# Kernel optimization log

Measured on AMD Instinct MI355X. Metric: run time of the kernel, lower is better.

## Reference

```python
import jax, jax.numpy as jnp
import numpy as np

HIDDEN = 512
HEADS = 8
HEAD_DIM = HIDDEN // HEADS  # 64
NUM_FEATURES = 256
EPS = 1e-4


def _gaussian_orthogonal_random_matrix(num_rows, num_cols, scaling=0, seed=1234):
    """Blocks of orthogonal rows from QR of gaussian matrices, rescaled (FAVOR+)."""
    rng = np.random.default_rng(seed)
    blocks = []
    full_blocks = num_rows // num_cols
    for _ in range(full_blocks):
        q, _ = np.linalg.qr(rng.standard_normal((num_cols, num_cols)))
        blocks.append(q.T)
    rem = num_rows - full_blocks * num_cols
    if rem > 0:
        q, _ = np.linalg.qr(rng.standard_normal((num_cols, num_cols)))
        blocks.append(q.T[:rem])
    mat = np.concatenate(blocks, axis=0)  # [num_rows, num_cols]
    if scaling == 0:
        # row norms of a fresh gaussian matrix (chi-distributed multipliers)
        multiplier = np.linalg.norm(rng.standard_normal((num_rows, num_cols)), axis=1)
    else:
        multiplier = np.sqrt(num_cols) * np.ones(num_rows)
    return (multiplier[:, None] * mat).astype(np.float32)


def _split_heads(x, b):
    # [b, n, hidden] -> [b, h, n, head_dim]
    return x.reshape(b, -1, HEADS, HEAD_DIM).transpose(0, 2, 1, 3)


def _phi(data, proj):
    """Nonnegative softmax kernel feature map (FAVOR+).
    data: [b,h,n,d], proj: [m,d] -> [b,h,n,m]"""
    d = data.shape[-1]
    m = proj.shape[0]
    x = data * (d ** -0.25)
    dash = jnp.einsum('bhnd,md->bhnm', x, proj)
    diag = 0.5 * jnp.sum(x * x, axis=-1, keepdims=True)
    return (m ** -0.5) * jnp.exp(dash - diag) + EPS


def setup_inputs() -> dict:
    key = jax.random.key(0)
    ks = jax.random.split(key, 12)
    b, n = 2, 8192
    s = HIDDEN ** -0.5
    inp = {
        'query': jax.random.normal(ks[0], (b, n, HIDDEN), jnp.float32),
        'key':   jax.random.normal(ks[1], (b, n, HIDDEN), jnp.float32),
        'value': jax.random.normal(ks[2], (b, n, HIDDEN), jnp.float32),
        'WQ_w': jax.random.normal(ks[3], (HIDDEN, HIDDEN), jnp.float32) * s,
        'WQ_b': jnp.zeros((HIDDEN,), jnp.float32),
        'WK_w': jax.random.normal(ks[4], (HIDDEN, HIDDEN), jnp.float32) * s,
        'WK_b': jnp.zeros((HIDDEN,), jnp.float32),
        'WV_w': jax.random.normal(ks[5], (HIDDEN, HIDDEN), jnp.float32) * s,
        'WV_b': jnp.zeros((HIDDEN,), jnp.float32),
        'WO_w': jax.random.normal(ks[6], (HIDDEN, HIDDEN), jnp.float32) * s,
        'WO_b': jnp.zeros((HIDDEN,), jnp.float32),
        'proj': jnp.asarray(_gaussian_orthogonal_random_matrix(NUM_FEATURES, HEAD_DIM)),
    }
    return inp


def reference(query, key, value, WQ_w, WQ_b, WK_w, WK_b, WV_w, WV_b, WO_w, WO_b, proj):
    b = query.shape[0]
    # torch Linear: y = x @ W.T + b
    Q = _split_heads(jnp.einsum('bnd,ed->bne', query, WQ_w) + WQ_b, b)
    K = _split_heads(jnp.einsum('bnd,ed->bne', key,   WK_w) + WK_b, b)
    V = _split_heads(jnp.einsum('bnd,ed->bne', value, WV_w) + WV_b, b)

    Qp = _phi(Q, proj)  # [b,h,n,m]
    Kp = _phi(K, proj)  # [b,h,n,m]

    # denominator: Q' @ sum_n K'  -> [b,h,n,1]
    denom = jnp.einsum('bhnm,bhm->bhn', Qp, jnp.sum(Kp, axis=2))[..., None]
    # linear attention: Q' @ (K'^T V), O(n*m*d)
    ctx = jnp.einsum('bhnm,bhnd->bhmd', Kp, V)
    attn = jnp.einsum('bhnm,bhmd->bhnd', Qp, ctx) / denom

    # faithful to original: .view(batch, -1, hidden) directly on [b,h,n,d]
    attn = attn.reshape(b, -1, HIDDEN)
    return jnp.einsum('bnd,ed->bne', attn, WO_w) + WO_b
```

## Files before the change

kernel.cpp:

```cpp
#include <hip/hip_runtime.h>

typedef __attribute__((ext_vector_type(8))) _Float16 f16x8;
typedef __attribute__((ext_vector_type(4))) float f32x4;

#define S4 0.35355339059327373f

static __device__ __forceinline__ ushort f2h(float f) {
  return __builtin_bit_cast(ushort, (_Float16)f);
}

static __device__ __forceinline__ void gload16(const void* g, void* l) {
  __builtin_amdgcn_global_load_lds((const __attribute__((address_space(1))) void*)g,
                                   (__attribute__((address_space(3))) void*)l, 16, 0, 0);
}

static __device__ __forceinline__ void cvt_store8(ushort* dst, float4 a, float4 b) {
  f16x8 h;
  h[0] = (_Float16)a.x; h[1] = (_Float16)a.y; h[2] = (_Float16)a.z; h[3] = (_Float16)a.w;
  h[4] = (_Float16)b.x; h[5] = (_Float16)b.y; h[6] = (_Float16)b.z; h[7] = (_Float16)b.w;
  *(f16x8*)dst = h;
}

template<int BM, int BN, int WR, int WC, int EPI, int ZMODE, int DIAG, int AF32, int BF32>
__global__ __launch_bounds__(256) void gemm_bt(
    const void* __restrict__ Av, const void* __restrict__ Bv,
    const float* __restrict__ bias, ushort* __restrict__ Cb,
    float* __restrict__ Cf, const float* __restrict__ rv0,
    float* __restrict__ dg,
    int K, int ldA, int ldB, int ldC, int Mz,
    long sAz, long sBz, long sCz)
{
  constexpr int BK = 32;
  constexpr int WTM = BM / WR, WTN = BN / WC;
  constexpr int MI = WTM / 16, NI = WTN / 16;
  constexpr int LDSB = (BM + BN) * 64;

  __shared__ uint4 smem4[LDSB / 16];
  char* smem = (char*)smem4;
  ushort* As = (ushort*)smem;
  ushort* Bs = (ushort*)(smem + BM * 64);

  const int tid = threadIdx.x;
  const int l = tid & 63, w = tid >> 6;
  const int wr = w / WC, wc = w % WC;
  const int lr = l & 15, lk = l >> 4;
  const int tm = blockIdx.x * BM, tn = blockIdx.y * BN;
  const int z = blockIdx.z;

  const ushort* Ah = (const ushort*)Av;
  const ushort* Bh = (const ushort*)Bv;
  const float*  Af = (const float*)Av;
  const float*  Bf = (const float*)Bv;
  long aoff = 0, boff = 0;
  if (ZMODE == 0) { aoff = (long)z * sAz; boff = (long)z * sBz; }
  if (ZMODE == 1) { aoff = (long)(z >> 3) * sAz + (z & 7) * 64; boff = (long)z * sBz; }
  Ah += aoff; Bh += boff; Af += aoff; Bf += boff;
  const float* rv = (EPI == 1) ? (rv0 + (long)z * Mz) : nullptr;
  const long coff = (long)z * sCz;

  f32x4 acc[MI][NI];
#pragma unroll
  for (int i = 0; i < MI; ++i)
#pragma unroll
    for (int j = 0; j < NI; ++j) acc[i][j] = f32x4{0.f, 0.f, 0.f, 0.f};

  for (int k0 = 0; k0 < K; k0 += BK) {
    if constexpr (AF32) {
      const int ar = tid >> 1, ac = (tid & 1) * 16;
      const float* g = Af + (long)(tm + ar) * ldA + k0 + ac;
      float4 f0 = *(const float4*)(g);
      float4 f1 = *(const float4*)(g + 4);
      float4 f2 = *(const float4*)(g + 8);
      float4 f3 = *(const float4*)(g + 12);
      cvt_store8(As + ar * 32 + ac, f0, f1);
      cvt_store8(As + ar * 32 + ac + 8, f2, f3);
    } else {
      constexpr int AB = BM * 64;
#pragma unroll
      for (int s = 0; s < (AB + 4095) / 4096; ++s) {
        const int base = s * 4096 + w * 1024;
        if (base < AB) {
          const int idx = base + l * 16;
          gload16(Ah + (long)(tm + (idx >> 6)) * ldA + k0 + ((idx & 63) >> 1),
                  (char*)As + base);
        }
      }
    }
    if constexpr (BF32) {
      const int br = tid >> 1, bc = (tid & 1) * 16;
      const float* g = Bf + (long)(tn + br) * ldB + k0 + bc;
      float4 f0 = *(const float4*)(g);
      float4 f1 = *(const float4*)(g + 4);
      float4 f2 = *(const float4*)(g + 8);
      float4 f3 = *(const float4*)(g + 12);
      cvt_store8(Bs + br * 32 + bc, f0, f1);
      cvt_store8(Bs + br * 32 + bc + 8, f2, f3);
    } else {
      constexpr int BB = BN * 64;
#pragma unroll
      for (int s = 0; s < (BB + 4095) / 4096; ++s) {
        const int base = s * 4096 + w * 1024;
        if (base < BB) {
          const int idx = base + l * 16;
          gload16(Bh + (long)(tn + (idx >> 6)) * ldB + k0 + ((idx & 63) >> 1),
                  (char*)Bs + base);
        }
      }
    }
    __syncthreads();

    f16x8 af[MI], bfr[NI];
#pragma unroll
    for (int mi = 0; mi < MI; ++mi)
      af[mi] = *(const f16x8*)(As + (wr * WTM + mi * 16 + lr) * 32 + lk * 8);
#pragma unroll
    for (int ni = 0; ni < NI; ++ni)
      bfr[ni] = *(const f16x8*)(Bs + (wc * WTN + ni * 16 + lr) * 32 + lk * 8);
#pragma unroll
    for (int mi = 0; mi < MI; ++mi)
#pragma unroll
      for (int ni = 0; ni < NI; ++ni)
        acc[mi][ni] = __builtin_amdgcn_mfma_f32_16x16x32_f16(af[mi], bfr[ni], acc[mi][ni], 0, 0, 0);
    __syncthreads();
  }

#pragma unroll
  for (int mi = 0; mi < MI; ++mi) {
#pragma unroll
    for (int j = 0; j < 4; ++j) {
      const int row = tm + wr * WTM + mi * 16 + lk * 4 + j;
      float ds = 0.f;
#pragma unroll
      for (int ni = 0; ni < NI; ++ni) {
        const int col = tn + wc * WTN + ni * 16 + lr;
        float v = acc[mi][ni][j];
        if (EPI == 0 || EPI == 3) v += bias[col];
        if (EPI == 4) v += bias[row];
        if (EPI == 1) v = 0.0625f * __expf(v - rv[row]) + 1e-4f;
        if (DIAG) ds += v * v;
        if (EPI == 4) {
          const int b = col >> 13, nn = col & 8191;
          const int h = row >> 6, d = row & 63;
          Cb[(long)(b * 8 + h) * 655360 + (long)d * 8192 + nn] = f2h(v);
        } else if (EPI == 3) {
          Cf[coff + (long)row * ldC + col] = v;
        } else {
          Cb[coff + (long)row * ldC + col] = f2h(v);
        }
      }
      if (DIAG) {
        ds += __shfl_xor(ds, 1, 64);
        ds += __shfl_xor(ds, 2, 64);
        ds += __shfl_xor(ds, 4, 64);
        ds += __shfl_xor(ds, 8, 64);
        if (lr == 0) {
          const int b = row >> 13, nn = row & 8191;
          const int head = (tn + wc * WTN) >> 6;
          dg[(long)(b * 8 + head) * 8192 + nn] = 0.0625f * ds;
        }
      }
    }
  }
}

__global__ __launch_bounds__(256) void phictx_k(
    const ushort* __restrict__ Kh, const ushort* __restrict__ Vt,
    const ushort* __restrict__ pjh, const float* __restrict__ diagK,
    float* __restrict__ cpart)
{
  const int by = blockIdx.x, z = blockIdx.y;
  const int kc = z >> 4, bh = z & 15;
  const int b = bh >> 3, h = bh & 7;
  const int n0c = kc * 1024;
  const int tid = threadIdx.x, l = tid & 63, w = tid >> 6;
  const int lr = l & 15, lk = l >> 4;

  __shared__ char smem[39680];
  ushort* Pj = (ushort*)smem;
  ushort* Ks = (ushort*)(smem + 18432);
  ushort* Vs = (ushort*)(smem + 23040);
  ushort* Kp = (ushort*)(smem + 29440);

  {
    const ushort* src = pjh + by * 128 * 64;
#pragma unroll
    for (int c = tid; c < 1024; c += 256) {
      const int row = c >> 3, cole = (c & 7) * 8;
      *(uint4*)(Pj + row * 72 + cole) = *(const uint4*)(src + row * 64 + cole);
    }
  }
  const ushort* KB = Kh + (long)b * 4194304 + h * 64;
  const ushort* VB = Vt + (long)bh * 655360;
  const float* rv = diagK + (long)bh * 8192;

  f32x4 acc[5][2];
#pragma unroll
  for (int i = 0; i < 5; ++i) {
    acc[i][0] = f32x4{0.f, 0.f, 0.f, 0.f};
    acc[i][1] = f32x4{0.f, 0.f, 0.f, 0.f};
  }

  for (int ns = 0; ns < 32; ++ns) {
    const int n0 = n0c + ns * 32;
    {
      const int row = tid >> 3, cole = (tid & 7) * 8;
      uint4 u = *(const uint4*)(KB + (long)(n0 + row) * 512 + cole);
      *(uint4*)(Ks + row * 72 + cole) = u;
    }
    {
#pragma unroll
      for (int c = tid; c < 320; c += 256) {
        const int row = c >> 2, cole = (c & 3) * 8;
        uint4 u = *(const uint4*)(VB + (long)row * 8192 + n0 + cole);
        *(uint4*)(Vs + row * 40 + cole) = u;
      }
    }
    __syncthreads();

    f32x4 a2[2][2];
    a2[0][0] = f32x4{0.f,0.f,0.f,0.f}; a2[0][1] = f32x4{0.f,0.f,0.f,0.f};
    a2[1][0] = f32x4{0.f,0.f,0.f,0.f}; a2[1][1] = f32x4{0.f,0.f,0.f,0.f};
#pragma unroll
    for (int kk = 0; kk < 2; ++kk) {
      f16x8 pa[2], kb[2];
#pragma unroll
      for (int mi = 0; mi < 2; ++mi)
        pa[mi] = *(const f16x8*)(Pj + (w * 32 + mi * 16 + lr) * 72 + kk * 32 + lk * 8);
#pragma unroll
      for (int ni = 0; ni < 2; ++ni)
        kb[ni] = *(const f16x8*)(Ks + (ni * 16 + lr) * 72 + kk * 32 + lk * 8);
#pragma unroll
      for (int mi = 0; mi < 2; ++mi)
#pragma unroll
        for (int ni = 0; ni < 2; ++ni)
          a2[mi][ni] = __builtin_amdgcn_mfma_f32_16x16x32_f16(pa[mi], kb[ni], a2[mi][ni], 0, 0, 0);
    }
#pragma unroll
    for (int mi = 0; mi < 2; ++mi)
#pragma unroll
      for (int ni = 0; ni < 2; ++ni)
#pragma unroll
        for (int j = 0; j < 4; ++j) {
          const int mrow = w * 32 + mi * 16 + lk * 4 + j;
          const int ncol = ni * 16 + lr;
          const float vv = 0.0625f * __expf(a2[mi][ni][j] - rv[n0 + ncol]) + 1e-4f;
          Kp[mrow * 40 + ncol] = f2h(vv);
        }
    __syncthreads();

    f16x8 va[5], kb2[2];
#pragma unroll
    for (int mi = 0; mi < 5; ++mi)
      va[mi] = *(const f16x8*)(Vs + (mi * 16 + lr) * 40 + lk * 8);
#pragma unroll
    for (int ni = 0; ni < 2; ++ni)
      kb2[ni] = *(const f16x8*)(Kp + (w * 32 + ni * 16 + lr) * 40 + lk * 8);
#pragma unroll
    for (int mi = 0; mi < 5; ++mi)
#pragma unroll
      for (int ni = 0; ni < 2; ++ni)
        acc[mi][ni] = __builtin_amdgcn_mfma_f32_16x16x32_f16(va[mi], kb2[ni], acc[mi][ni], 0, 0, 0);
    __syncthreads();
  }

  float* out = cpart + (long)z * 20480;
#pragma unroll
  for (int mi = 0; mi < 5; ++mi)
#pragma unroll
    for (int ni = 0; ni < 2; ++ni)
#pragma unroll
      for (int j = 0; j < 4; ++j) {
        const int row = mi * 16 + lk * 4 + j;
        const int col = by * 128 + w * 32 + ni * 16 + lr;
        out[(long)row * 256 + col] = acc[mi][ni][j];
      }
}

__global__ __launch_bounds__(256) void phiattn_k(
    const ushort* __restrict__ Qh, const ushort* __restrict__ pjh,
    const float* __restrict__ diagQ, const ushort* __restrict__ ctxb,
    ushort* __restrict__ attnR)
{
  const int bx = blockIdx.x, bh = blockIdx.y;
  const int b = bh >> 3, h = bh & 7;
  const int tm = bx * 128;
  const int tid = threadIdx.x, l = tid & 63, w = tid >> 6;
  const int lr = l & 15, lk = l >> 4;
  const int wr = w >> 1, wc = w & 1;

  __shared__ char smem[126208];
  ushort* P  = (ushort*)smem;
  ushort* Cs = (ushort*)(smem + 67584);
  ushort* As = (ushort*)(smem + 109824);
  ushort* Bs = (ushort*)(smem + 118016);

  {
    const ushort* cb = ctxb + (long)bh * 20480;
#pragma unroll
    for (int c = tid; c < 2560; c += 256) {
      const int row = c >> 5, cole = (c & 31) * 8;
      *(uint4*)(Cs + row * 264 + cole) = *(const uint4*)(cb + row * 256 + cole);
    }
  }
  const ushort* QB = Qh + (long)b * 4194304 + h * 64;
  const float* rv = diagQ + (long)bh * 8192;

  for (int nh = 0; nh < 2; ++nh) {
    const ushort* PB = pjh + nh * 8192;
    f32x4 a2[4][4];
#pragma unroll
    for (int i = 0; i < 4; ++i)
#pragma unroll
      for (int j = 0; j < 4; ++j) a2[i][j] = f32x4{0.f, 0.f, 0.f, 0.f};

    for (int k0 = 0; k0 < 64; k0 += 32) {
#pragma unroll
      for (int s = 0; s < 2; ++s) {
        const int base = s * 4096 + w * 1024;
        const int idx = base + l * 16;
        gload16(QB + (long)(tm + (idx >> 6)) * 512 + k0 + ((idx & 63) >> 1),
                (char*)As + base);
      }
#pragma unroll
      for (int s = 0; s < 2; ++s) {
        const int base = s * 4096 + w * 1024;
        const int idx = base + l * 16;
        gload16(PB + (long)(idx >> 6) * 64 + k0 + ((idx & 63) >> 1),
                (char*)Bs + base);
      }
      __syncthreads();
      f16x8 af[4], bfr[4];
#pragma unroll
      for (int mi = 0; mi < 4; ++mi)
        af[mi] = *(const f16x8*)(As + (wr * 64 + mi * 16 + lr) * 32 + lk * 8);
#pragma unroll
      for (int ni = 0; ni < 4; ++ni)
        bfr[ni] = *(const f16x8*)(Bs + (wc * 64 + ni * 16 + lr) * 32 + lk * 8);
#pragma unroll
      for (int mi = 0; mi < 4; ++mi)
#pragma unroll
        for (int ni = 0; ni < 4; ++ni)
          a2[mi][ni] = __builtin_amdgcn_mfma_f32_16x16x32_f16(af[mi], bfr[ni], a2[mi][ni], 0, 0, 0);
      __syncthreads();
    }
#pragma unroll
    for (int mi = 0; mi < 4; ++mi)
#pragma unroll
      for (int ni = 0; ni < 4; ++ni)
#pragma unroll
        for (int j = 0; j < 4; ++j) {
          const int row = wr * 64 + mi * 16 + lk * 4 + j;
          const int col = nh * 128 + wc * 64 + ni * 16 + lr;
          const float vv = 0.0625f * __expf(a2[mi][ni][j] - rv[tm + row]) + 1e-4f;
          P[row * 264 + col] = f2h(vv);
        }
  }
  __syncthreads();

  f32x4 acc[2][5];
#pragma unroll
  for (int i = 0; i < 2; ++i)
#pragma unroll
    for (int j = 0; j < 5; ++j) acc[i][j] = f32x4{0.f, 0.f, 0.f, 0.f};

  for (int k0 = 0; k0 < 256; k0 += 32) {
    f16x8 pa[2], cbf[5];
#pragma unroll
    for (int mi = 0; mi < 2; ++mi)
      pa[mi] = *(const f16x8*)(P + (w * 32 + mi * 16 + lr) * 264 + k0 + lk * 8);
#pragma unroll
    for (int ni = 0; ni < 5; ++ni)
      cbf[ni] = *(const f16x8*)(Cs + (ni * 16 + lr) * 264 + k0 + lk * 8);
#pragma unroll
    for (int mi = 0; mi < 2; ++mi)
#pragma unroll
      for (int ni = 0; ni < 5; ++ni)
        acc[mi][ni] = __builtin_amdgcn_mfma_f32_16x16x32_f16(pa[mi], cbf[ni], acc[mi][ni], 0, 0, 0);
  }

  ushort* outb = attnR + (long)bh * 524288;
#pragma unroll
  for (int mi = 0; mi < 2; ++mi)
#pragma unroll
    for (int j = 0; j < 4; ++j) {
      const float dv = __shfl(acc[mi][4][j], (l & 48), 64);
      const int row = tm + w * 32 + mi * 16 + lk * 4 + j;
#pragma unroll
      for (int ni = 0; ni < 4; ++ni) {
        const int col = ni * 16 + lr;
        outb[(long)row * 64 + col] = f2h(acc[mi][ni][j] / dv);
      }
    }
}

__global__ void cvt_k(const float* __restrict__ in, ushort* __restrict__ out,
                      int n4, float scale) {
  int i = blockIdx.x * blockDim.x + threadIdx.x;
  if (i >= n4) return;
  float4 v = ((const float4*)in)[i];
  ushort4 o;
  o.x = f2h(v.x * scale); o.y = f2h(v.y * scale);
  o.z = f2h(v.z * scale); o.w = f2h(v.w * scale);
  ((ushort4*)out)[i] = o;
}

__global__ __launch_bounds__(256) void vtpad_k(ushort* __restrict__ Vt) {
  const int i = blockIdx.x * 256 + threadIdx.x;
  const int bh = i >> 14, rem = i & 16383, r = rem >> 10, n8 = rem & 1023;
  const unsigned val = (r == 0) ? 0x3C003C00u : 0u;
  uint4 u; u.x = val; u.y = val; u.z = val; u.w = val;
  *(uint4*)(Vt + (long)bh * 655360 + (long)(64 + r) * 8192 + n8 * 8) = u;
}

__global__ __launch_bounds__(256) void ctxred_k(const float* __restrict__ cp,
                                                ushort* __restrict__ ctxb) {
  const int idx = blockIdx.x * 256 + threadIdx.x;
  const int bh = idx / 20480, rem = idx % 20480;
  float a = 0.f;
#pragma unroll
  for (int kc = 0; kc < 8; ++kc) a += cp[(long)(kc * 16 + bh) * 20480 + rem];
  ctxb[idx] = f2h(a);
}

extern "C" void kernel_launch(void* const* d_in, const int* in_sizes, int n_in,
                              void* d_out, int out_size, void* d_ws, size_t ws_size,
                              hipStream_t stream) {
  (void)in_sizes; (void)n_in; (void)out_size; (void)ws_size;
  const float* q  = (const float*)d_in[0];
  const float* k  = (const float*)d_in[1];
  const float* v  = (const float*)d_in[2];
  const float* wq = (const float*)d_in[3];
  const float* bq = (const float*)d_in[4];
  const float* wk = (const float*)d_in[5];
  const float* bk = (const float*)d_in[6];
  const float* wv = (const float*)d_in[7];
  const float* bv = (const float*)d_in[8];
  const float* wo = (const float*)d_in[9];
  const float* bo = (const float*)d_in[10];
  const float* pj = (const float*)d_in[11];

  char* ws = (char*)d_ws;
  ushort* attnR = (ushort*)(ws + 0);
  float*  cpart = (float*)(ws + 16777216);
  ushort* wqh   = (ushort*)(ws + 27262976);
  ushort* wkh   = (ushort*)(ws + 27787264);
  ushort* wvh   = (ushort*)(ws + 28311552);
  ushort* woh   = (ushort*)(ws + 28835840);
  ushort* pjh   = (ushort*)(ws + 29360128);
  ushort* Qh    = (ushort*)(ws + 29392896);
  ushort* Kh    = (ushort*)(ws + 46170112);
  ushort* Vt    = (ushort*)(ws + 62947328);
  float*  diagQ = (float*)(ws + 83918848);
  float*  diagK = (float*)(ws + 84443136);
  ushort* ctxb  = (ushort*)(ws + 84967424);

  cvt_k<<<256, 256, 0, stream>>>(wq, wqh, 65536, 1.f);
  cvt_k<<<256, 256, 0, stream>>>(wk, wkh, 65536, 1.f);
  cvt_k<<<256, 256, 0, stream>>>(wv, wvh, 65536, 1.f);
  cvt_k<<<256, 256, 0, stream>>>(wo, woh, 65536, 1.f);
  cvt_k<<<16, 256, 0, stream>>>(pj, pjh, 4096, S4);
  vtpad_k<<<1024, 256, 0, stream>>>(Vt);

  gemm_bt<128,128,2,2,0,0,1,1,0><<<dim3(128,4,1), 256, 0, stream>>>(
      q, wqh, bq, Qh, nullptr, nullptr, diagQ, 512, 512, 512, 512, 0, 0L, 0L, 0L);
  gemm_bt<128,128,2,2,0,0,1,1,0><<<dim3(128,4,1), 256, 0, stream>>>(
      k, wkh, bk, Kh, nullptr, nullptr, diagK, 512, 512, 512, 512, 0, 0L, 0L, 0L);

  gemm_bt<128,128,2,2,4,0,0,0,1><<<dim3(4,128,1), 256, 0, stream>>>(
      wvh, v, bv, Vt, nullptr, nullptr, nullptr, 512, 512, 512, 0, 0, 0L, 0L, 0L);

  phictx_k<<<dim3(2,128), 256, 0, stream>>>(Kh, Vt, pjh, diagK, cpart);
  ctxred_k<<<1280, 256, 0, stream>>>(cpart, ctxb);

  phiattn_k<<<dim3(64,16), 256, 0, stream>>>(Qh, pjh, diagQ, ctxb, attnR);

  gemm_bt<128,128,2,2,3,0,0,0,0><<<dim3(128,4,1), 256, 0, stream>>>(
      attnR, woh, bo, nullptr, (float*)d_out, nullptr, nullptr, 512, 512, 512, 512, 0,
      0L, 0L, 0L);
}
```

Before: 210.0 us.

## Split fused phi-K/context kernel into two generic GEMMs via materialized K-features

After: 201.8 us. 3.9% less time.

```diff
diff --git a/kernel.cpp b/kernel.cpp
--- a/kernel.cpp
+++ b/kernel.cpp
@@ -53,9 +53,13 @@
   const float*  Bf = (const float*)Bv;
   long aoff = 0, boff = 0;
   if (ZMODE == 0) { aoff = (long)z * sAz; boff = (long)z * sBz; }
-  if (ZMODE == 1) { aoff = (long)(z >> 3) * sAz + (z & 7) * 64; boff = (long)z * sBz; }
+  if (ZMODE == 2) { aoff = (long)z * sAz; boff = (long)(z >> 3) * sBz + (z & 7) * 64; }
+  if (ZMODE == 3) {
+    aoff = (long)(z & 15) * sAz + (long)(z >> 4) * 1024;
+    boff = (long)(z & 15) * sBz + (long)(z >> 4) * 1024;
+  }
   Ah += aoff; Bh += boff; Af += aoff; Bf += boff;
-  const float* rv = (EPI == 1) ? (rv0 + (long)z * Mz) : nullptr;
+  const float* rv = (EPI == 6) ? (rv0 + (long)z * Mz) : nullptr;
   const long coff = (long)z * sCz;
 
   f32x4 acc[MI][NI];
@@ -136,13 +140,13 @@
         float v = acc[mi][ni][j];
         if (EPI == 0 || EPI == 3) v += bias[col];
         if (EPI == 4) v += bias[row];
-        if (EPI == 1) v = 0.0625f * __expf(v - rv[row]) + 1e-4f;
+        if (EPI == 6) v = 0.0625f * __expf(v - rv[col]) + 1e-4f;
         if (DIAG) ds += v * v;
         if (EPI == 4) {
           const int b = col >> 13, nn = col & 8191;
           const int h = row >> 6, d = row & 63;
           Cb[(long)(b * 8 + h) * 655360 + (long)d * 8192 + nn] = f2h(v);
-        } else if (EPI == 3) {
+        } else if (EPI == 3 || EPI == 5) {
           Cf[coff + (long)row * ldC + col] = v;
         } else {
           Cb[coff + (long)row * ldC + col] = f2h(v);
@@ -161,119 +165,6 @@
       }
     }
   }
-}
-
-__global__ __launch_bounds__(256) void phictx_k(
-    const ushort* __restrict__ Kh, const ushort* __restrict__ Vt,
-    const ushort* __restrict__ pjh, const float* __restrict__ diagK,
-    float* __restrict__ cpart)
-{
-  const int by = blockIdx.x, z = blockIdx.y;
-  const int kc = z >> 4, bh = z & 15;
-  const int b = bh >> 3, h = bh & 7;
-  const int n0c = kc * 1024;
-  const int tid = threadIdx.x, l = tid & 63, w = tid >> 6;
-  const int lr = l & 15, lk = l >> 4;
-
-  __shared__ char smem[39680];
-  ushort* Pj = (ushort*)smem;
-  ushort* Ks = (ushort*)(smem + 18432);
-  ushort* Vs = (ushort*)(smem + 23040);
-  ushort* Kp = (ushort*)(smem + 29440);
-
-  {
-    const ushort* src = pjh + by * 128 * 64;
-#pragma unroll
-    for (int c = tid; c < 1024; c += 256) {
-      const int row = c >> 3, cole = (c & 7) * 8;
-      *(uint4*)(Pj + row * 72 + cole) = *(const uint4*)(src + row * 64 + cole);
-    }
-  }
-  const ushort* KB = Kh + (long)b * 4194304 + h * 64;
-  const ushort* VB = Vt + (long)bh * 655360;
-  const float* rv = diagK + (long)bh * 8192;
-
-  f32x4 acc[5][2];
-#pragma unroll
-  for (int i = 0; i < 5; ++i) {
-    acc[i][0] = f32x4{0.f, 0.f, 0.f, 0.f};
-    acc[i][1] = f32x4{0.f, 0.f, 0.f, 0.f};
-  }
-
-  for (int ns = 0; ns < 32; ++ns) {
-    const int n0 = n0c + ns * 32;
-    {
-      const int row = tid >> 3, cole = (tid & 7) * 8;
-      uint4 u = *(const uint4*)(KB + (long)(n0 + row) * 512 + cole);
-      *(uint4*)(Ks + row * 72 + cole) = u;
-    }
-    {
-#pragma unroll
-      for (int c = tid; c < 320; c += 256) {
-        const int row = c >> 2, cole = (c & 3) * 8;
-        uint4 u = *(const uint4*)(VB + (long)row * 8192 + n0 + cole);
-        *(uint4*)(Vs + row * 40 + cole) = u;
-      }
-    }
-    __syncthreads();
-
-    f32x4 a2[2][2];
-    a2[0][0] = f32x4{0.f,0.f,0.f,0.f}; a2[0][1] = f32x4{0.f,0.f,0.f,0.f};
-    a2[1][0] = f32x4{0.f,0.f,0.f,0.f}; a2[1][1] = f32x4{0.f,0.f,0.f,0.f};
-#pragma unroll
-    for (int kk = 0; kk < 2; ++kk) {
-      f16x8 pa[2], kb[2];
-#pragma unroll
-      for (int mi = 0; mi < 2; ++mi)
-        pa[mi] = *(const f16x8*)(Pj + (w * 32 + mi * 16 + lr) * 72 + kk * 32 + lk * 8);
-#pragma unroll
-      for (int ni = 0; ni < 2; ++ni)
-        kb[ni] = *(const f16x8*)(Ks + (ni * 16 + lr) * 72 + kk * 32 + lk * 8);
-#pragma unroll
-      for (int mi = 0; mi < 2; ++mi)
-#pragma unroll
-        for (int ni = 0; ni < 2; ++ni)
-          a2[mi][ni] = __builtin_amdgcn_mfma_f32_16x16x32_f16(pa[mi], kb[ni], a2[mi][ni], 0, 0, 0);
-    }
-#pragma unroll
-    for (int mi = 0; mi < 2; ++mi)
-#pragma unroll
-      for (int ni = 0; ni < 2; ++ni)
-#pragma unroll
-        for (int j = 0; j < 4; ++j) {
-          const int mrow = w * 32 + mi * 16 + lk * 4 + j;
-          const int ncol = ni * 16 + lr;
-          const float vv = 0.0625f * __expf(a2[mi][ni][j] - rv[n0 + ncol]) + 1e-4f;
-          Kp[mrow * 40 + ncol] = f2h(vv);
-        }
-    __syncthreads();
-
-    f16x8 va[5], kb2[2];
-#pragma unroll
-    for (int mi = 0; mi < 5; ++mi)
-      va[mi] = *(const f16x8*)(Vs + (mi * 16 + lr) * 40 + lk * 8);
-#pragma unroll
-    for (int ni = 0; ni < 2; ++ni)
-      kb2[ni] = *(const f16x8*)(Kp + (w * 32 + ni * 16 + lr) * 40 + lk * 8);
-#pragma unroll
-    for (int mi = 0; mi < 5; ++mi)
-#pragma unroll
-      for (int ni = 0; ni < 2; ++ni)
-        acc[mi][ni] = __builtin_amdgcn_mfma_f32_16x16x32_f16(va[mi], kb2[ni], acc[mi][ni], 0, 0, 0);
-    __syncthreads();
-  }
-
-  float* out = cpart + (long)z * 20480;
-#pragma unroll
-  for (int mi = 0; mi < 5; ++mi)
-#pragma unroll
-    for (int ni = 0; ni < 2; ++ni)
-#pragma unroll
-      for (int j = 0; j < 4; ++j) {
-        const int row = mi * 16 + lk * 4 + j;
-        const int col = by * 128 + w * 32 + ni * 16 + lr;
-        out[(long)row * 256 + col] = acc[mi][ni][j];
-      }
 }
 
 __global__ __launch_bounds__(256) void phiattn_k(
@@ -393,15 +284,27 @@
     }
 }
 
-__global__ void cvt_k(const float* __restrict__ in, ushort* __restrict__ out,
-                      int n4, float scale) {
-  int i = blockIdx.x * blockDim.x + threadIdx.x;
-  if (i >= n4) return;
-  float4 v = ((const float4*)in)[i];
+__global__ __launch_bounds__(256) void cvtall_k(
+    const float* __restrict__ wq, const float* __restrict__ wk,
+    const float* __restrict__ wv, const float* __restrict__ wo,
+    const float* __restrict__ pj,
+    ushort* __restrict__ wqh, ushort* __restrict__ wkh,
+    ushort* __restrict__ wvh, ushort* __restrict__ woh,
+    ushort* __restrict__ pjh)
+{
+  int i = blockIdx.x * 256 + threadIdx.x;
+  const float* in; ushort* out; float scale = 1.f; int idx;
+  if (i < 65536)       { in = wq; out = wqh; idx = i; }
+  else if (i < 131072) { in = wk; out = wkh; idx = i - 65536; }
+  else if (i < 196608) { in = wv; out = wvh; idx = i - 131072; }
+  else if (i < 262144) { in = wo; out = woh; idx = i - 196608; }
+  else if (i < 266240) { in = pj; out = pjh; idx = i - 262144; scale = S4; }
+  else return;
+  float4 v = ((const float4*)in)[idx];
   ushort4 o;
   o.x = f2h(v.x * scale); o.y = f2h(v.y * scale);
   o.z = f2h(v.z * scale); o.w = f2h(v.w * scale);
-  ((ushort4*)out)[i] = o;
+  ((ushort4*)out)[idx] = o;
 }
 
 __global__ __launch_bounds__(256) void vtpad_k(ushort* __restrict__ Vt) {
@@ -450,15 +353,12 @@
   ushort* Qh    = (ushort*)(ws + 29392896);
   ushort* Kh    = (ushort*)(ws + 46170112);
   ushort* Vt    = (ushort*)(ws + 62947328);
-  float*  diagQ = (float*)(ws + 83918848);
-  float*  diagK = (float*)(ws + 84443136);
-  ushort* ctxb  = (ushort*)(ws + 84967424);
-
-  cvt_k<<<256, 256, 0, stream>>>(wq, wqh, 65536, 1.f);
-  cvt_k<<<256, 256, 0, stream>>>(wk, wkh, 65536, 1.f);
-  cvt_k<<<256, 256, 0, stream>>>(wv, wvh, 65536, 1.f);
-  cvt_k<<<256, 256, 0, stream>>>(wo, woh, 65536, 1.f);
-  cvt_k<<<16, 256, 0, stream>>>(pj, pjh, 4096, S4);
+  ushort* KpT   = (ushort*)(ws + 83918848);
+  float*  diagQ = (float*)(ws + 151027712);
+  float*  diagK = (float*)(ws + 151552000);
+  ushort* ctxb  = (ushort*)(ws + 152076288);
+
+  cvtall_k<<<1040, 256, 0, stream>>>(wq, wk, wv, wo, pj, wqh, wkh, wvh, woh, pjh);
   vtpad_k<<<1024, 256, 0, stream>>>(Vt);
 
   gemm_bt<128,128,2,2,0,0,1,1,0><<<dim3(128,4,1), 256, 0, stream>>>(
@@ -469,7 +369,13 @@
   gemm_bt<128,128,2,2,4,0,0,0,1><<<dim3(4,128,1), 256, 0, stream>>>(
       wvh, v, bv, Vt, nullptr, nullptr, nullptr, 512, 512, 512, 0, 0, 0L, 0L, 0L);
 
-  phictx_k<<<dim3(2,128), 256, 0, stream>>>(Kh, Vt, pjh, diagK, cpart);
+  gemm_bt<128,128,2,2,6,2,0,0,0><<<dim3(2,64,16), 256, 0, stream>>>(
+      pjh, Kh, nullptr, KpT, nullptr, diagK, nullptr, 64, 64, 512, 8192, 8192,
+      0L, 4194304L, 2097152L);
+
+  gemm_bt<80,128,1,4,5,3,0,0,0><<<dim3(1,2,128), 256, 0, stream>>>(
+      Vt, KpT, nullptr, nullptr, cpart, nullptr, nullptr, 1024, 8192, 8192, 256, 0,
+      655360L, 2097152L, 20480L);
   ctxred_k<<<1280, 256, 0, stream>>>(cpart, ctxb);
 
   phiattn_k<<<dim3(64,16), 256, 0, stream>>>(Qh, pjh, diagQ, ctxb, attnR);
```
